# Kernel optimization log

Hardware: AMD Instinct MI355X
Metric: run time of the kernel (lower is better)

## Reference

```python
import jax, jax.numpy as jnp
import numpy as np

HIDDEN = 4096
N_HEADS = 32
N_KV_HEADS = 8
HEAD_DIM = 128
MAX_POS = 4096
N_GROUPS = N_HEADS // N_KV_HEADS  # 4


def _sincos_table():
    # create_sinusoidal_positions(MAX_POS, HEAD_DIM) -> [MAX_POS, 1, 2*HEAD_DIM]
    inv_freq = 1.0 / 10000 ** (np.arange(0, HEAD_DIM, 2) / HEAD_DIM)
    freqs = np.einsum('i,j->ij', np.arange(MAX_POS), inv_freq).astype('float32')
    emb = np.concatenate((freqs, freqs), axis=-1)  # [MAX_POS, HEAD_DIM]
    out = np.concatenate((np.sin(emb)[:, None, :], np.cos(emb)[:, None, :]), axis=-1)
    return jnp.asarray(out[:, :, :MAX_POS])  # slice is a no-op since 2*HEAD_DIM < MAX_POS

_SINCOS = _sincos_table()


def _rotate_half(t):
    half = t.shape[-1] // 2
    return jnp.concatenate((-t[..., half:], t[..., :half]), axis=-1)


def setup_inputs() -> dict:
    key = jax.random.key(0)
    ks = jax.random.split(key, 9)
    B, S = 1, 2048
    scale = 0.02
    return {
        'hidden_states': jax.random.normal(ks[0], (B, S, HIDDEN), jnp.float32),
        'attention_mask': jnp.ones((B, 1, 1, S), jnp.bool_),
        'position_ids': jnp.broadcast_to(jnp.arange(S, dtype=jnp.int32)[None, :], (B, S)),
        'Wq': jax.random.normal(ks[1], (HIDDEN, N_HEADS * HEAD_DIM), jnp.float32) * scale,
        'bq': jnp.zeros((N_HEADS * HEAD_DIM,), jnp.float32),
        'Wk': jax.random.normal(ks[2], (HIDDEN, N_KV_HEADS * HEAD_DIM), jnp.float32) * scale,
        'bk': jnp.zeros((N_KV_HEADS * HEAD_DIM,), jnp.float32),
        'Wv': jax.random.normal(ks[3], (HIDDEN, N_KV_HEADS * HEAD_DIM), jnp.float32) * scale,
        'bv': jnp.zeros((N_KV_HEADS * HEAD_DIM,), jnp.float32),
        'Wo': jax.random.normal(ks[4], (N_HEADS * HEAD_DIM, HIDDEN), jnp.float32) * scale,
        'bo': jnp.zeros((HIDDEN,), jnp.float32),
    }


def reference(hidden_states, attention_mask, position_ids, Wq, bq, Wk, bk, Wv, bv, Wo, bo):
    B, S, _ = hidden_states.shape
    # QKV projections + split heads
    q = (hidden_states @ Wq + bq).reshape(B, S, N_HEADS, HEAD_DIM)
    k = (hidden_states @ Wk + bk).reshape(B, S, N_KV_HEADS, HEAD_DIM)
    v = (hidden_states @ Wv + bv).reshape(B, S, N_KV_HEADS, HEAD_DIM)
    # Rotary embedding: sincos[position_ids] -> [B,S,1,2*HEAD_DIM]
    sincos = _SINCOS[position_ids]
    sin_pos, cos_pos = jnp.split(sincos, 2, axis=-1)  # each [B,S,1,HEAD_DIM]
    k = k * cos_pos + _rotate_half(k) * sin_pos
    q = q * cos_pos + _rotate_half(q) * sin_pos
    # Causal mask combined with padding mask
    causal = jnp.tril(jnp.ones((S, S), jnp.bool_))[None, None]  # [1,1,S,S]
    mask = jnp.logical_and(attention_mask, causal)  # [B,1,S,S]
    # GQA: repeat kv heads
    k = jnp.repeat(k, N_GROUPS, axis=2)  # [B,S,H,D]
    v = jnp.repeat(v, N_GROUPS, axis=2)
    bias = jnp.where(mask, 0.0, jnp.finfo(jnp.float32).min).astype(jnp.float32)
    scores = jnp.einsum('bqhd,bkhd->bhqk', q, k) / jnp.sqrt(jnp.float32(HEAD_DIM)) + bias
    attn_weights = jax.nn.softmax(scores, axis=-1)  # [B,H,S,S]
    attn_output = jnp.einsum('bhqk,bkhd->bqhd', attn_weights, v).reshape(B, S, N_HEADS * HEAD_DIM)
    return attn_output @ Wo + bo
```

## Files before the change

### kernel.cpp

```cpp
#include <hip/hip_runtime.h>
#include <hip/hip_bf16.h>
#include <math.h>

typedef __bf16 bf16x8 __attribute__((ext_vector_type(8)));
typedef __bf16 bf16x4 __attribute__((ext_vector_type(4)));
typedef float  f32x4  __attribute__((ext_vector_type(4)));
typedef unsigned int u32;

#define S_LEN 2048
#define HID   4096
#define NH    32
#define NKV   8
#define HD    128

__device__ inline void gld_lds16(const __bf16* g, __bf16* l) {
  __builtin_amdgcn_global_load_lds((const __attribute__((address_space(1))) u32*)g,
                                   (__attribute__((address_space(3))) u32*)l,
                                   16, 0, 0);
}

__global__ void cast_bf16(const float* __restrict__ in, __bf16* __restrict__ out, int n4) {
  int i = blockIdx.x * blockDim.x + threadIdx.x;
  if (i < n4) {
    float4 v = ((const float4*)in)[i];
    bf16x4 o;
    o[0] = (__bf16)v.x; o[1] = (__bf16)v.y; o[2] = (__bf16)v.z; o[3] = (__bf16)v.w;
    ((bf16x4*)out)[i] = o;
  }
}

template <typename T>
__global__ void transpose_cast(const T* __restrict__ in, __bf16* __restrict__ out,
                               int ldi, int ldo) {
  __shared__ float tile[32][33];
  const int c0 = blockIdx.x * 32, r0 = blockIdx.y * 32;
  const int tx = threadIdx.x, ty = threadIdx.y;
  for (int j = 0; j < 32; j += 8)
    tile[ty + j][tx] = (float)in[(size_t)(r0 + ty + j) * ldi + c0 + tx];
  __syncthreads();
  for (int j = 0; j < 32; j += 8)
    out[(size_t)(c0 + ty + j) * ldo + r0 + tx] = (__bf16)tile[tx][ty + j];
}

__global__ void concat_bias(const float* __restrict__ bk, const float* __restrict__ bv,
                            float* __restrict__ out) {
  int i = blockIdx.x * blockDim.x + threadIdx.x;
  if (i < 2048) out[i] = (i < 1024) ? bk[i] : bv[i - 1024];
}

template <typename CT>
__global__ __launch_bounds__(256) void gemm_bt(const __bf16* __restrict__ A,
                                               const __bf16* __restrict__ Bt,
                                               const float* __restrict__ bias,
                                               CT* __restrict__ C,
                                               int M, int N, int K) {
  __shared__ __bf16 As[128 * 64];
  __shared__ __bf16 Bs[128 * 64];
  const int tid  = threadIdx.x;
  const int lane = tid & 63;
  const int lrow = lane & 15, quad = lane >> 4;
  const int wave = tid >> 6;
  const int wm = (wave & 1) * 64, wn = (wave >> 1) * 64;
  const int m0 = blockIdx.y * 128, n0 = blockIdx.x * 128;

  f32x4 acc[4][4] = {};

  const __bf16* aP[4];
  const __bf16* bP[4];
  __bf16* aL[4];
  __bf16* bL[4];
#pragma unroll
  for (int s = 0; s < 4; s++) {
    const int c = tid + 256 * s;
    const int row = c >> 3;
    const int kc = ((c & 7) + row) & 7;
    aP[s] = A + (size_t)(m0 + row) * K + kc * 8;
    bP[s] = Bt + (size_t)(n0 + row) * K + kc * 8;
    aL[s] = As + c * 8;
    bL[s] = Bs + c * 8;
  }

  int offA[2][4], offB[2][4];
#pragma unroll
  for (int h = 0; h < 2; h++)
#pragma unroll
    for (int t = 0; t < 4; t++) {
      const int ra = wm + t * 16 + lrow;
      const int rb = wn + t * 16 + lrow;
      offA[h][t] = (ra * 8 + ((h * 4 + quad - ra) & 7)) * 8;
      offB[h][t] = (rb * 8 + ((h * 4 + quad - rb) & 7)) * 8;
    }

  for (int k0 = 0; k0 < K; k0 += 64) {
    __syncthreads();
#pragma unroll
    for (int s = 0; s < 4; s++) {
      gld_lds16(aP[s] + k0, aL[s]);
      gld_lds16(bP[s] + k0, bL[s]);
    }
    __syncthreads();

#pragma unroll
    for (int h = 0; h < 2; h++) {
      bf16x8 af[4], bfr[4];
#pragma unroll
      for (int t = 0; t < 4; t++) {
        af[t]  = *(const bf16x8*)(As + offA[h][t]);
        bfr[t] = *(const bf16x8*)(Bs + offB[h][t]);
      }
#pragma unroll
      for (int i = 0; i < 4; i++)
#pragma unroll
        for (int j = 0; j < 4; j++)
          acc[i][j] = __builtin_amdgcn_mfma_f32_16x16x32_bf16(af[i], bfr[j], acc[i][j], 0, 0, 0);
    }
  }

#pragma unroll
  for (int i = 0; i < 4; i++) {
    const int row = m0 + wm + i * 16 + quad * 4;
#pragma unroll
    for (int j = 0; j < 4; j++) {
      const int col = n0 + wn + j * 16 + lrow;
      const float b = bias[col];
#pragma unroll
      for (int r = 0; r < 4; r++)
        C[(size_t)(row + r) * N + col] = (CT)(acc[i][j][r] + b);
    }
  }
}

__global__ void rope_inplace(__bf16* __restrict__ Q, __bf16* __restrict__ KV,
                             const int* __restrict__ pos_ids) {
  const int s = blockIdx.y;
  const int t = blockIdx.x * blockDim.x + threadIdx.x;
  const int h = t >> 6, j = t & 63;
  const float pos = (float)pos_ids[s];
  const float inv_freq = __builtin_exp2f((float)j * -0.2076205059304601f);
  const float ang = pos * inv_freq;
  float sn, cs;
  sincosf(ang, &sn, &cs);
  if (h < NH) {
    __bf16* p = Q + (size_t)s * HID + h * HD + j;
    const float x0 = (float)p[0], x1 = (float)p[64];
    p[0]  = (__bf16)(x0 * cs - x1 * sn);
    p[64] = (__bf16)(x1 * cs + x0 * sn);
  } else {
    const int hk = h - NH;
    __bf16* p = KV + (size_t)s * 2048 + hk * HD + j;
    const float x0 = (float)p[0], x1 = (float)p[64];
    p[0]  = (__bf16)(x0 * cs - x1 * sn);
    p[64] = (__bf16)(x1 * cs + x0 * sn);
  }
}

__global__ __launch_bounds__(256) void flash_attn(const __bf16* __restrict__ Qb,
                                                  const __bf16* __restrict__ Kb,
                                                  const __bf16* __restrict__ Vt,
                                                  __bf16* __restrict__ attn, int ldk) {
  __shared__ __bf16 Ks[2][32 * 128];
  __shared__ __bf16 Vs[2][128 * 32];
  __shared__ __bf16 Plds[4][2][16][40];
  const int tid  = threadIdx.x;
  const int wave = tid >> 6;
  const int lane = tid & 63;
  const int lrow = lane & 15, quad = lane >> 4;

  const int c = blockIdx.x & 255, p = blockIdx.x >> 8;
  const int h = c >> 3;
  const int xh = c & 7;
  const int xx = p ? xh : 15 - xh;
  const int bq0 = xx * 128;
  const int kvh = h >> 2;
  const int T0 = bq0 + wave * 16;
  const int T1 = T0 + 64;
  const int kend = bq0 + 128;

  const __bf16* kg[2];
  const __bf16* vg[2];
  int kL[2], vL[2];
#pragma unroll
  for (int s = 0; s < 2; s++) {
    const int ck = tid + 256 * s;
    const int key = ck >> 4, kcb = ((ck & 15) + key) & 15;
    kg[s] = Kb + (size_t)key * ldk + kvh * HD + kcb * 8;
    kL[s] = ck * 8;
    const int d = ck >> 2, vcb = ((ck & 3) - (d >> 1)) & 3;
    vg[s] = Vt + (size_t)(kvh * HD + d) * S_LEN + vcb * 8;
    vL[s] = ck * 8;
  }

  int offK0[4], offK1[4], offV[8];
#pragma unroll
  for (int kc = 0; kc < 4; kc++) {
    const int rot = (kc * 4 + quad - lrow) & 15;
    offK0[kc] = (lrow * 16 + rot) * 8;
    offK1[kc] = ((lrow + 16) * 16 + rot) * 8;
  }
#pragma unroll
  for (int dt = 0; dt < 8; dt++) {
    const int d = dt * 16 + lrow;
    offV[dt] = (d * 4 + ((quad + (d >> 1)) & 3)) * 8;
  }

  bf16x8 qf[2][4];
#pragma unroll
  for (int m = 0; m < 2; m++) {
    const __bf16* qbase = Qb + (size_t)(T0 + m * 64 + lrow) * HID + h * HD + quad * 8;
#pragma unroll
    for (int kc = 0; kc < 4; kc++) qf[m][kc] = *(const bf16x8*)(qbase + kc * 32);
  }

  f32x4 o[2][8] = {};
  f32x4 lac[2] = {};
  bf16x8 ones;
#pragma unroll
  for (int j = 0; j < 8; j++) ones[j] = (__bf16)1.0f;

  const float cs = 0.08838834764831845f * 1.44269504088896f;

#pragma unroll
  for (int s = 0; s < 2; s++) {
    gld_lds16(kg[s], &Ks[0][0] + kL[s]);
    gld_lds16(vg[s], &Vs[0][0] + vL[s]);
  }

  int cur = 0;
  for (int kb = 0; kb < kend; kb += 32) {
    __syncthreads();
    if (kb + 32 < kend) {
      const int nxt = cur ^ 1;
#pragma unroll
      for (int s = 0; s < 2; s++) {
        gld_lds16(kg[s] + (size_t)(kb + 32) * ldk, &Ks[nxt][0] + kL[s]);
        gld_lds16(vg[s] + (kb + 32), &Vs[nxt][0] + vL[s]);
      }
    }

    bf16x8 kf0[4], kf1[4];
#pragma unroll
    for (int kc = 0; kc < 4; kc++) {
      kf0[kc] = *(const bf16x8*)(&Ks[cur][offK0[kc]]);
      kf1[kc] = *(const bf16x8*)(&Ks[cur][offK1[kc]]);
    }
    f32x4 s[2][2] = {};
#pragma unroll
    for (int kc = 0; kc < 4; kc++) {
      s[0][0] = __builtin_amdgcn_mfma_f32_16x16x32_bf16(qf[0][kc], kf0[kc], s[0][0], 0, 0, 0);
      s[0][1] = __builtin_amdgcn_mfma_f32_16x16x32_bf16(qf[0][kc], kf1[kc], s[0][1], 0, 0, 0);
      s[1][0] = __builtin_amdgcn_mfma_f32_16x16x32_bf16(qf[1][kc], kf0[kc], s[1][0], 0, 0, 0);
      s[1][1] = __builtin_amdgcn_mfma_f32_16x16x32_bf16(qf[1][kc], kf1[kc], s[1][1], 0, 0, 0);
    }
#pragma unroll
    for (int m = 0; m < 2; m++) {
      const int Tm = m ? T1 : T0;
#pragma unroll
      for (int n = 0; n < 2; n++) {
        const int col = kb + n * 16 + lrow;
#pragma unroll
        for (int r = 0; r < 4; r++) {
          const int row = Tm + quad * 4 + r;
          const float pv = (col <= row) ? __builtin_exp2f(s[m][n][r] * cs) : 0.0f;
          Plds[wave][m][quad * 4 + r][n * 16 + lrow] = (__bf16)pv;
        }
      }
    }
    bf16x8 pf0 = *(const bf16x8*)(&Plds[wave][0][lrow][quad * 8]);
    bf16x8 pf1 = *(const bf16x8*)(&Plds[wave][1][lrow][quad * 8]);
#pragma unroll
    for (int dt = 0; dt < 8; dt++) {
      bf16x8 vf = *(const bf16x8*)(&Vs[cur][offV[dt]]);
      o[0][dt] = __builtin_amdgcn_mfma_f32_16x16x32_bf16(pf0, vf, o[0][dt], 0, 0, 0);
      o[1][dt] = __builtin_amdgcn_mfma_f32_16x16x32_bf16(pf1, vf, o[1][dt], 0, 0, 0);
    }
    lac[0] = __builtin_amdgcn_mfma_f32_16x16x32_bf16(pf0, ones, lac[0], 0, 0, 0);
    lac[1] = __builtin_amdgcn_mfma_f32_16x16x32_bf16(pf1, ones, lac[1], 0, 0, 0);
    cur ^= 1;
  }

#pragma unroll
  for (int m = 0; m < 2; m++) {
    const int Tm = m ? T1 : T0;
#pragma unroll
    for (int r = 0; r < 4; r++) {
      const float inv_l = 1.0f / lac[m][r];
      const size_t rowoff = (size_t)(Tm + quad * 4 + r) * HID + h * HD;
#pragma unroll
      for (int dt = 0; dt < 8; dt++)
        attn[rowoff + dt * 16 + lrow] = (__bf16)(o[m][dt][r] * inv_l);
    }
  }
}

extern "C" void kernel_launch(void* const* d_in, const int* in_sizes, int n_in,
                              void* d_out, int out_size, void* d_ws, size_t ws_size,
                              hipStream_t stream) {
  const float* hs = (const float*)d_in[0];
  const int* pos = (const int*)d_in[2];
  const float* Wq = (const float*)d_in[3];
  const float* bq = (const float*)d_in[4];
  const float* Wk = (const float*)d_in[5];
  const float* bk = (const float*)d_in[6];
  const float* Wv = (const float*)d_in[7];
  const float* bv = (const float*)d_in[8];
  const float* Wo = (const float*)d_in[9];
  const float* bo = (const float*)d_in[10];
  float* out = (float*)d_out;
  char* ws = (char*)d_ws;
  char* oc = (char*)d_out;

  __bf16* bHS   = (__bf16*)(ws + 0);
  __bf16* bWT   = (__bf16*)(ws + ((size_t)16 << 20));
  __bf16* bAttn = bHS;
  __bf16* bQ   = (__bf16*)(oc + 0);
  __bf16* bKV  = (__bf16*)(oc + ((size_t)16 << 20));
  __bf16* bVt  = (__bf16*)(oc + ((size_t)24 << 20));
  float*  bKVb = (float*)(oc + ((size_t)28 << 20));

  dim3 tb(32, 8);

  cast_bf16<<<8192, 256, 0, stream>>>(hs, bHS, (S_LEN * HID) / 4);
  transpose_cast<float><<<dim3(128, 128), tb, 0, stream>>>(Wq, bWT, 4096, 4096);
  gemm_bt<__bf16><<<dim3(32, 16), 256, 0, stream>>>(bHS, bWT, bq, bQ, 2048, 4096, 4096);
  transpose_cast<float><<<dim3(32, 128), tb, 0, stream>>>(Wk, bWT, 1024, 4096);
  transpose_cast<float><<<dim3(32, 128), tb, 0, stream>>>(Wv, bWT + (size_t)1024 * 4096, 1024, 4096);
  concat_bias<<<8, 256, 0, stream>>>(bk, bv, bKVb);
  gemm_bt<__bf16><<<dim3(16, 16), 256, 0, stream>>>(bHS, bWT, bKVb, bKV, 2048, 2048, 4096);
  rope_inplace<<<dim3(10, 2048), 256, 0, stream>>>(bQ, bKV, pos);
  transpose_cast<__bf16><<<dim3(32, 64), tb, 0, stream>>>(bKV + 1024, bVt, 2048, 2048);
  flash_attn<<<512, 256, 0, stream>>>(bQ, bKV, bVt, bAttn, 2048);
  transpose_cast<float><<<dim3(128, 128), tb, 0, stream>>>(Wo, bWT, 4096, 4096);
  gemm_bt<float><<<dim3(32, 16), 256, 0, stream>>>(bAttn, bWT, bo, out, 2048, 4096, 4096);
}
```

Measured before the change: 565.7 us.

## Keep attention probabilities in registers via transposed QK MFMA and permuted V layout

Swaps the operand order of the QK^T MFMA so that each lane's score outputs already match the A-operand layout needed for the PV MFMA. This removes the per-wave LDS round trip for the probability tile (the Plds write and read-back). To make the key ordering line up, V is transposed with a permutation of key indices within each 32-block. This removes the LDS traffic and the wait between the softmax and PV steps in the attention inner loop. The V transpose kernel now computes a permuted store index.

Measured after the change: 559.3 us. About the same (-1.1%).

```diff
diff --git a/kernel.cpp b/kernel.cpp
--- a/kernel.cpp
+++ b/kernel.cpp
@@ -40,6 +40,19 @@
   __syncthreads();
   for (int j = 0; j < 32; j += 8)
     out[(size_t)(c0 + ty + j) * ldo + r0 + tx] = (__bf16)tile[tx][ty + j];
+}
+
+__global__ void transpose_cast_vperm(const __bf16* __restrict__ in, __bf16* __restrict__ out,
+                                     int ldi, int ldo) {
+  __shared__ float tile[32][33];
+  const int c0 = blockIdx.x * 32, r0 = blockIdx.y * 32;
+  const int tx = threadIdx.x, ty = threadIdx.y;
+  for (int j = 0; j < 32; j += 8)
+    tile[ty + j][tx] = (float)in[(size_t)(r0 + ty + j) * ldi + c0 + tx];
+  __syncthreads();
+  const int sx = ((tx >> 2) & 3) * 8 + ((tx >> 4) & 1) * 4 + (tx & 3);
+  for (int j = 0; j < 32; j += 8)
+    out[(size_t)(c0 + ty + j) * ldo + r0 + sx] = (__bf16)tile[tx][ty + j];
 }
 
 __global__ void concat_bias(const float* __restrict__ bk, const float* __restrict__ bv,
@@ -160,7 +173,6 @@
                                                   __bf16* __restrict__ attn, int ldk) {
   __shared__ __bf16 Ks[2][32 * 128];
   __shared__ __bf16 Vs[2][128 * 32];
-  __shared__ __bf16 Plds[4][2][16][40];
   const int tid  = threadIdx.x;
   const int wave = tid >> 6;
   const int lane = tid & 63;
@@ -246,35 +258,32 @@
     f32x4 s[2][2] = {};
 #pragma unroll
     for (int kc = 0; kc < 4; kc++) {
-      s[0][0] = __builtin_amdgcn_mfma_f32_16x16x32_bf16(qf[0][kc], kf0[kc], s[0][0], 0, 0, 0);
-      s[0][1] = __builtin_amdgcn_mfma_f32_16x16x32_bf16(qf[0][kc], kf1[kc], s[0][1], 0, 0, 0);
-      s[1][0] = __builtin_amdgcn_mfma_f32_16x16x32_bf16(qf[1][kc], kf0[kc], s[1][0], 0, 0, 0);
-      s[1][1] = __builtin_amdgcn_mfma_f32_16x16x32_bf16(qf[1][kc], kf1[kc], s[1][1], 0, 0, 0);
-    }
+      s[0][0] = __builtin_amdgcn_mfma_f32_16x16x32_bf16(kf0[kc], qf[0][kc], s[0][0], 0, 0, 0);
+      s[0][1] = __builtin_amdgcn_mfma_f32_16x16x32_bf16(kf1[kc], qf[0][kc], s[0][1], 0, 0, 0);
+      s[1][0] = __builtin_amdgcn_mfma_f32_16x16x32_bf16(kf0[kc], qf[1][kc], s[1][0], 0, 0, 0);
+      s[1][1] = __builtin_amdgcn_mfma_f32_16x16x32_bf16(kf1[kc], qf[1][kc], s[1][1], 0, 0, 0);
+    }
+    bf16x8 pf[2];
 #pragma unroll
     for (int m = 0; m < 2; m++) {
-      const int Tm = m ? T1 : T0;
-#pragma unroll
-      for (int n = 0; n < 2; n++) {
-        const int col = kb + n * 16 + lrow;
+      const int qrow = (m ? T1 : T0) + lrow;
+#pragma unroll
+      for (int n = 0; n < 2; n++)
 #pragma unroll
         for (int r = 0; r < 4; r++) {
-          const int row = Tm + quad * 4 + r;
-          const float pv = (col <= row) ? __builtin_exp2f(s[m][n][r] * cs) : 0.0f;
-          Plds[wave][m][quad * 4 + r][n * 16 + lrow] = (__bf16)pv;
+          const int key = kb + n * 16 + quad * 4 + r;
+          const float pv = (key <= qrow) ? __builtin_exp2f(s[m][n][r] * cs) : 0.0f;
+          pf[m][n * 4 + r] = (__bf16)pv;
         }
-      }
-    }
-    bf16x8 pf0 = *(const bf16x8*)(&Plds[wave][0][lrow][quad * 8]);
-    bf16x8 pf1 = *(const bf16x8*)(&Plds[wave][1][lrow][quad * 8]);
+    }
 #pragma unroll
     for (int dt = 0; dt < 8; dt++) {
       bf16x8 vf = *(const bf16x8*)(&Vs[cur][offV[dt]]);
-      o[0][dt] = __builtin_amdgcn_mfma_f32_16x16x32_bf16(pf0, vf, o[0][dt], 0, 0, 0);
-      o[1][dt] = __builtin_amdgcn_mfma_f32_16x16x32_bf16(pf1, vf, o[1][dt], 0, 0, 0);
-    }
-    lac[0] = __builtin_amdgcn_mfma_f32_16x16x32_bf16(pf0, ones, lac[0], 0, 0, 0);
-    lac[1] = __builtin_amdgcn_mfma_f32_16x16x32_bf16(pf1, ones, lac[1], 0, 0, 0);
+      o[0][dt] = __builtin_amdgcn_mfma_f32_16x16x32_bf16(pf[0], vf, o[0][dt], 0, 0, 0);
+      o[1][dt] = __builtin_amdgcn_mfma_f32_16x16x32_bf16(pf[1], vf, o[1][dt], 0, 0, 0);
+    }
+    lac[0] = __builtin_amdgcn_mfma_f32_16x16x32_bf16(pf[0], ones, lac[0], 0, 0, 0);
+    lac[1] = __builtin_amdgcn_mfma_f32_16x16x32_bf16(pf[1], ones, lac[1], 0, 0, 0);
     cur ^= 1;
   }
 
@@ -327,7 +336,7 @@
   concat_bias<<<8, 256, 0, stream>>>(bk, bv, bKVb);
   gemm_bt<__bf16><<<dim3(16, 16), 256, 0, stream>>>(bHS, bWT, bKVb, bKV, 2048, 2048, 4096);
   rope_inplace<<<dim3(10, 2048), 256, 0, stream>>>(bQ, bKV, pos);
-  transpose_cast<__bf16><<<dim3(32, 64), tb, 0, stream>>>(bKV + 1024, bVt, 2048, 2048);
+  transpose_cast_vperm<<<dim3(32, 64), tb, 0, stream>>>(bKV + 1024, bVt, 2048, 2048);
   flash_attn<<<512, 256, 0, stream>>>(bQ, bKV, bVt, bAttn, 2048);
   transpose_cast<float><<<dim3(128, 128), tb, 0, stream>>>(Wo, bWT, 4096, 4096);
   gemm_bt<float><<<dim3(32, 16), 256, 0, stream>>>(bAttn, bWT, bo, out, 2048, 4096, 4096);
```
